# Optimization experiments

Measured on AMD Instinct MI355X. Metric: run time of the kernel, lower is better.

Reference implementation:

```python
import jax, jax.numpy as jnp
import numpy as np

N_NODES = 50000
N_EDGES = 600000
D = 128
N_LAYERS = 4  # 2 base + 2 resnet layers
N_GRAPHS = 64
NEG_SLOPE = 0.01  # F.leaky_relu default


def setup_inputs() -> dict:
    key = jax.random.key(0)
    k1, k2, k3, k4, k5 = jax.random.split(key, 5)
    x = jax.random.normal(k1, (N_NODES, D), dtype=jnp.float32)
    edge_index = jax.random.randint(k2, (2, N_EDGES), 0, N_NODES, dtype=jnp.int64)
    batch = jnp.sort(jax.random.randint(k3, (N_NODES,), 0, N_GRAPHS, dtype=jnp.int64))
    Wl = jax.random.normal(k4, (N_LAYERS, D, D), dtype=jnp.float32) * 0.05
    bl = jnp.zeros((N_LAYERS, D), dtype=jnp.float32)
    Wr = jax.random.normal(k5, (N_LAYERS, D, D), dtype=jnp.float32) * 0.05
    return {"x": x, "edge_index": edge_index, "batch": batch,
            "Wl": Wl, "bl": bl, "Wr": Wr}


def _mean_aggregate(x, src, dst, n_nodes):
    # mean over incoming neighbors; isolated nodes get 0 (PyG scatter-mean semantics)
    s = jax.ops.segment_sum(x[src], dst, num_segments=n_nodes)  # [N, D]
    cnt = jax.ops.segment_sum(jnp.ones((src.shape[0],), x.dtype), dst,
                              num_segments=n_nodes)
    return s / jnp.maximum(cnt, 1.0)[:, None]


def reference(x, edge_index, batch, Wl, bl, Wr):
    src, dst = edge_index[0], edge_index[1]
    n = x.shape[0]
    for i in range(N_LAYERS):
        agg = _mean_aggregate(x, src, dst, n)                      # [N, D]
        # SAGEConv: lin_l(agg) + lin_r(x); lin_l has bias, lin_r does not
        x_new = agg @ Wl[i].T + bl[i] + x @ Wr[i].T
        x_new = jnp.where(x_new >= 0, x_new, NEG_SLOPE * x_new)    # leaky_relu
        x = x_new if i < 2 else x + x_new                          # residual after first 2
    # global mean pool per graph
    pooled = jax.ops.segment_sum(x, batch, num_segments=N_GRAPHS)  # [G, D]
    counts = jax.ops.segment_sum(jnp.ones((n,), x.dtype), batch,
                                 num_segments=N_GRAPHS)
    return pooled / jnp.maximum(counts, 1.0)[:, None]
```

## Files before the change

### kernel.cpp

```cpp
#include <hip/hip_runtime.h>

#define N_NODES 50000
#define N_EDGES 600000
#define DIM 128
#define N_LAYERS 4
#define N_GRAPHS 64
#define NEG_SLOPE 0.01f
#define NB_SCAN ((N_NODES + 255) / 256)
#define NB_CNT ((N_EDGES + 255) / 256)
#define NC_CONV (N_NODES * DIM / 8 / 256)
#define NB_PACK 64
#define RS 264

typedef __attribute__((ext_vector_type(8))) short short8;
typedef __attribute__((ext_vector_type(16))) float floatx16;

__device__ __forceinline__ unsigned short f2bf(float f) {
    union { float f; unsigned u; } c; c.f = f;
    unsigned u = c.u;
    unsigned r = (u + 0x7FFFu + ((u >> 16) & 1u)) >> 16;
    return (unsigned short)r;
}
__device__ __forceinline__ float bfraw2f(unsigned short b) {
    union { unsigned u; float f; } c; c.u = ((unsigned)b) << 16;
    return c.f;
}
__device__ __forceinline__ float bflo(unsigned u) {
    union { unsigned u; float f; } c; c.u = u << 16; return c.f;
}
__device__ __forceinline__ float bfhi(unsigned u) {
    union { unsigned u; float f; } c; c.u = u & 0xFFFF0000u; return c.f;
}

__global__ void zero2(int* a, int na, int* b, int nb) {
    int i = blockIdx.x * blockDim.x + threadIdx.x;
    if (i < na) a[i] = 0;
    else if (i < na + nb) b[i - na] = 0;
}

__global__ void preprocess(const float4* __restrict__ x, uint4* __restrict__ xb,
                           const float* __restrict__ Wl, const float* __restrict__ Wr,
                           ushort* __restrict__ wpk,
                           const int* __restrict__ edst, int* __restrict__ deg) {
    int b = blockIdx.x;
    if (b < NC_CONV) {
        int i = b * 256 + threadIdx.x;
        float4 a = x[i * 2], c = x[i * 2 + 1];
        uint4 o;
        o.x = ((unsigned)f2bf(a.y) << 16) | f2bf(a.x);
        o.y = ((unsigned)f2bf(a.w) << 16) | f2bf(a.z);
        o.z = ((unsigned)f2bf(c.y) << 16) | f2bf(c.x);
        o.w = ((unsigned)f2bf(c.w) << 16) | f2bf(c.z);
        xb[i] = o;
    } else if (b < NC_CONV + NB_PACK) {
        int u = (b - NC_CONV) * 4 + (threadIdx.x >> 6);
        int l = threadIdx.x & 63;
        int layer = u >> 6, m = (u >> 5) & 1, s = (u >> 2) & 7, tt = u & 3;
        const float* W = ((m == 0) ? Wl : Wr) + (size_t)layer * DIM * DIM;
        int n = tt * 32 + (l & 31);
        int kb = s * 16 + (l >> 5) * 8;
        size_t off = ((size_t)u * 64 + l) * 8;
        for (int j = 0; j < 8; j++)
            wpk[off + j] = f2bf(W[n * DIM + kb + j]);
    } else {
        int e = (b - NC_CONV - NB_PACK) * 256 + threadIdx.x;
        if (e < N_EDGES) atomicAdd(&deg[edst[e]], 1);
    }
}

__global__ void scan_pass1(const int* __restrict__ deg, int* __restrict__ bsum) {
    int i = blockIdx.x * 256 + threadIdx.x;
    int v = (i < N_NODES) ? deg[i] : 0;
    for (int off = 32; off > 0; off >>= 1) v += __shfl_down(v, off, 64);
    __shared__ int ws[4];
    int lane = threadIdx.x & 63, w = threadIdx.x >> 6;
    if (lane == 0) ws[w] = v;
    __syncthreads();
    if (threadIdx.x == 0) bsum[blockIdx.x] = ws[0] + ws[1] + ws[2] + ws[3];
}

__global__ void scan_pass2(int* __restrict__ bsum) {
    __shared__ int sm[256];
    int t = threadIdx.x;
    int v = (t < NB_SCAN) ? bsum[t] : 0;
    sm[t] = v;
    __syncthreads();
    for (int off = 1; off < 256; off <<= 1) {
        int u = (t >= off) ? sm[t - off] : 0;
        __syncthreads();
        sm[t] += u;
        __syncthreads();
    }
    if (t < NB_SCAN) bsum[t] = sm[t] - v;
}

__global__ void scan_pass3(const int* __restrict__ deg, const int* __restrict__ bsum,
                           int* __restrict__ rp) {
    int i = blockIdx.x * 256 + threadIdx.x;
    int v = (i < N_NODES) ? deg[i] : 0;
    int lane = threadIdx.x & 63, w = threadIdx.x >> 6;
    int s = v;
    for (int off = 1; off < 64; off <<= 1) {
        int t = __shfl_up(s, off, 64);
        if (lane >= off) s += t;
    }
    __shared__ int ws[4];
    if (lane == 63) ws[w] = s;
    __syncthreads();
    int wo = 0;
    for (int k = 0; k < 4; k++) wo += (k < w) ? ws[k] : 0;
    int incl = s + wo + bsum[blockIdx.x];
    if (i < N_NODES) rp[i + 1] = incl;
    if (i == 0) rp[0] = 0;
}

__global__ void fill_gstart(const int* __restrict__ src, const int* __restrict__ dst,
                            const int* __restrict__ rp, int* __restrict__ fill,
                            int* __restrict__ csr,
                            const int* __restrict__ batch, int* __restrict__ gstart) {
    int b = blockIdx.x;
    if (b < NB_CNT) {
        int e = b * 256 + threadIdx.x;
        if (e >= N_EDGES) return;
        int d = dst[e];
        int pos = atomicAdd(&fill[d], 1);
        csr[rp[d] + pos] = src[e];
    } else {
        int i = (b - NB_CNT) * 256 + threadIdx.x;
        if (i >= N_NODES) return;
        int g0 = batch[i];
        if (i == 0) {
            for (int g = 0; g <= g0; g++) gstart[g] = 0;
        } else {
            int p = batch[i - 1];
            for (int g = p + 1; g <= g0; g++) gstart[g] = i;
        }
        if (i == N_NODES - 1) {
            for (int g = g0 + 1; g <= N_GRAPHS; g++) gstart[g] = N_NODES;
        }
    }
}

__global__ __launch_bounds__(256, 4) void fused_layer_mfma(
    const ushort* __restrict__ xin, ushort* __restrict__ xout,
    const int* __restrict__ rp, const int* __restrict__ csr,
    const ushort* __restrict__ wpk, const float* __restrict__ bias,
    const int* __restrict__ batch, float* __restrict__ pooled,
    int residual, int do_pool) {
    __shared__ ushort sA[64 * RS];
    int t = threadIdx.x;
    int node0 = blockIdx.x * 64;
    int w = t >> 6, l = t & 63;

    const uint4* xv = (const uint4*)(xin + (size_t)node0 * DIM);
#pragma unroll
    for (int i = 0; i < 4; i++) {
        int idx = t + i * 256;
        int r = idx >> 4, c = idx & 15;
        uint4 val = make_uint4(0u, 0u, 0u, 0u);
        if (node0 + r < N_NODES) val = xv[r * 16 + c];
        *(uint4*)&sA[r * RS + 128 + c * 8] = val;
    }

    {
        int ll = l & 15, eg = l >> 4;
        int nb = node0 + w * 16;
        int rpv = rp[min(nb + l, N_NODES)];
        const uint4* x16B = (const uint4*)xin;
        for (int i = 0; i < 16; i++) {
            int s = __shfl(rpv, i, 64);
            int e = __shfl(rpv, i + 1, 64);
            float a0 = 0.f, a1 = 0.f, a2 = 0.f, a3 = 0.f,
                  a4 = 0.f, a5 = 0.f, a6 = 0.f, a7 = 0.f;
            for (int base = s; base < e; base += 64) {
                int cnt = min(64, e - base);
                unsigned myidx = (base + l < e) ? (unsigned)csr[base + l] : 0u;
                for (int j = 0; j < cnt; j += 16) {
                    uint4 v[4];
#pragma unroll
                    for (int k = 0; k < 4; k++) {
                        int sel = j + k * 4 + eg;
                        unsigned idx = __shfl(myidx, sel, 64);
                        v[k] = make_uint4(0u, 0u, 0u, 0u);
                        if (sel < cnt) v[k] = x16B[(size_t)idx * 16 + ll];
                    }
#pragma unroll
                    for (int k = 0; k < 4; k++) {
                        a0 += bflo(v[k].x); a1 += bfhi(v[k].x);
                        a2 += bflo(v[k].y); a3 += bfhi(v[k].y);
                        a4 += bflo(v[k].z); a5 += bfhi(v[k].z);
                        a6 += bflo(v[k].w); a7 += bfhi(v[k].w);
                    }
                }
            }
            a0 += __shfl_xor(a0, 16, 64); a0 += __shfl_xor(a0, 32, 64);
            a1 += __shfl_xor(a1, 16, 64); a1 += __shfl_xor(a1, 32, 64);
            a2 += __shfl_xor(a2, 16, 64); a2 += __shfl_xor(a2, 32, 64);
            a3 += __shfl_xor(a3, 16, 64); a3 += __shfl_xor(a3, 32, 64);
            a4 += __shfl_xor(a4, 16, 64); a4 += __shfl_xor(a4, 32, 64);
            a5 += __shfl_xor(a5, 16, 64); a5 += __shfl_xor(a5, 32, 64);
            a6 += __shfl_xor(a6, 16, 64); a6 += __shfl_xor(a6, 32, 64);
            a7 += __shfl_xor(a7, 16, 64); a7 += __shfl_xor(a7, 32, 64);
            if (eg == 0) {
                float inv = 1.0f / (float)max(e - s, 1);
                uint4 o;
                o.x = ((unsigned)f2bf(a1 * inv) << 16) | f2bf(a0 * inv);
                o.y = ((unsigned)f2bf(a3 * inv) << 16) | f2bf(a2 * inv);
                o.z = ((unsigned)f2bf(a5 * inv) << 16) | f2bf(a4 * inv);
                o.w = ((unsigned)f2bf(a7 * inv) << 16) | f2bf(a6 * inv);
                *(uint4*)&sA[(w * 16 + i) * RS + ll * 8] = o;
            }
        }
    }
    __syncthreads();

    int m0 = (w >> 1) * 32;
    int th = w & 1;
    const ushort* arow = &sA[(m0 + (l & 31)) * RS];
    int khalf = (l >> 5) * 8;

    floatx16 acc0, acc1;
    for (int ii = 0; ii < 16; ii++) acc0[ii] = acc1[ii] = 0.f;

    const ushort* wl8 = wpk + (size_t)l * 8 + (size_t)(2 * th) * 512;
#pragma unroll
    for (int s2 = 0; s2 < 16; s2++) {
        int m = s2 >> 3, s = s2 & 7;
        short8 a = *(const short8*)(arow + m * 128 + s * 16 + khalf);
        size_t fb = (size_t)((m * 8 + s) * 4) * 512;
        short8 b0 = *(const short8*)(wl8 + fb);
        short8 b1 = *(const short8*)(wl8 + fb + 512);
        acc0 = __builtin_amdgcn_mfma_f32_32x32x16_bf16(a, b0, acc0, 0, 0, 0);
        acc1 = __builtin_amdgcn_mfma_f32_32x32x16_bf16(a, b1, acc1, 0, 0, 0);
    }

    int col = l & 31;
    int rbase = 4 * (l >> 5);
    floatx16 accs[2] = {acc0, acc1};
    if (!do_pool) {
#pragma unroll
        for (int ti = 0; ti < 2; ti++) {
            int n = (2 * th + ti) * 32 + col;
            float bv = bias[n];
#pragma unroll
            for (int r = 0; r < 16; r++) {
                int row = (r & 3) + 8 * (r >> 2) + rbase;
                int gm = m0 + row;
                int gn = node0 + gm;
                if (gn >= N_NODES) continue;
                float v = accs[ti][r] + bv;
                v = (v >= 0.f) ? v : NEG_SLOPE * v;
                if (residual) v += bfraw2f(sA[gm * RS + 128 + n]);
                xout[(size_t)gn * DIM + n] = f2bf(v);
            }
        }
    } else {
        bool fast = (node0 + 63 < N_NODES) && (batch[node0] == batch[node0 + 63]);
        int g0 = batch[node0];
#pragma unroll
        for (int ti = 0; ti < 2; ti++) {
            int n = (2 * th + ti) * 32 + col;
            float bv = bias[n];
            float psum = 0.f;
#pragma unroll
            for (int r = 0; r < 16; r++) {
                int row = (r & 3) + 8 * (r >> 2) + rbase;
                int gm = m0 + row;
                int gn = node0 + gm;
                if (gn >= N_NODES) continue;
                float v = accs[ti][r] + bv;
                v = (v >= 0.f) ? v : NEG_SLOPE * v;
                if (residual) v += bfraw2f(sA[gm * RS + 128 + n]);
                if (fast) psum += v;
                else atomicAdd(&pooled[batch[gn] * DIM + n], v);
            }
            if (fast) {
                psum += __shfl_xor(psum, 32, 64);
                if (l < 32) atomicAdd(&pooled[g0 * DIM + n], psum);
            }
        }
    }
}

__global__ void pool_final(const float* __restrict__ pooled,
                           const int* __restrict__ gstart,
                           float* __restrict__ out) {
    int i = blockIdx.x * blockDim.x + threadIdx.x;
    if (i >= N_GRAPHS * DIM) return;
    int g = i >> 7;
    int cnt = gstart[g + 1] - gstart[g];
    out[i] = pooled[i] / (float)max(cnt, 1);
}


extern "C" void kernel_launch(void* const* d_in, const int* in_sizes, int n_in,
                              void* d_out, int out_size, void* d_ws, size_t ws_size,
                              hipStream_t stream) {
    const float* x     = (const float*)d_in[0];
    const int*   ei    = (const int*)d_in[1];
    const int*   batch = (const int*)d_in[2];
    const float* Wl    = (const float*)d_in[3];
    const float* bl    = (const float*)d_in[4];
    const float* Wr    = (const float*)d_in[5];
    float* out = (float*)d_out;

    const int* esrc = ei;
    const int* edst = ei + N_EDGES;

    ushort* xb0  = (ushort*)d_ws;
    ushort* xbuf = xb0 + (size_t)N_NODES * DIM;
    ushort* agg  = xbuf + (size_t)N_NODES * DIM;
    ushort* wpk  = agg + (size_t)N_NODES * DIM;
    int* deg    = (int*)(wpk + (size_t)N_LAYERS * 2 * DIM * DIM);
    int* fill   = deg + N_NODES;
    int* csr    = fill + N_NODES;
    int* rp     = csr + N_EDGES;
    int* gstart = rp + (N_NODES + 1);
    int* bsum   = gstart + (N_GRAPHS + 1);
    float* pooled = (float*)(bsum + NB_SCAN);

    zero2<<<(2 * N_NODES + N_GRAPHS * DIM + 255) / 256, 256, 0, stream>>>(
        deg, 2 * N_NODES, (int*)pooled, N_GRAPHS * DIM);

    preprocess<<<NC_CONV + NB_PACK + NB_CNT, 256, 0, stream>>>(
        (const float4*)x, (uint4*)xb0, Wl, Wr, wpk, edst, deg);

    scan_pass1<<<NB_SCAN, 256, 0, stream>>>(deg, bsum);
    scan_pass2<<<1, 256, 0, stream>>>(bsum);
    scan_pass3<<<NB_SCAN, 256, 0, stream>>>(deg, bsum, rp);

    fill_gstart<<<NB_CNT + NB_SCAN, 256, 0, stream>>>(esrc, edst, rp, fill, csr,
                                                      batch, gstart);

    int gemm_blocks = (N_NODES + 63) / 64;
    const ushort* xi = xb0;
    ushort* xo = xbuf;
    for (int l = 0; l < N_LAYERS; l++) {
        fused_layer_mfma<<<gemm_blocks, 256, 0, stream>>>(
            xi, xo, rp, csr, wpk + (size_t)l * 2 * DIM * DIM,
            bl + (size_t)l * DIM, batch, pooled,
            (l >= 2) ? 1 : 0, (l == N_LAYERS - 1) ? 1 : 0);
        ushort* tmp = (ushort*)xi; xi = xo; xo = tmp;
    }

    pool_final<<<(N_GRAPHS * DIM + 255) / 256, 256, 0, stream>>>(pooled, gstart, out);
}
```

Before: 325.3 us.

## Split aggregation into feature-sliced gather kernel and store activations slice-major

Activations are stored in a feature-sliced layout of four 32-column slices, each contiguous across nodes. Neighbor aggregation moves to a separate kernel with one block per (node block, slice), so each gather touches a smaller working set that fits in cache better. The GEMM kernel then reads the precomputed aggregate and x from the sliced layout. This costs an extra launch per layer and a round trip of the aggregate through global memory, and gives up the fusion of gather and GEMM.

```diff
diff --git a/kernel.cpp b/kernel.cpp
--- a/kernel.cpp
+++ b/kernel.cpp
@@ -10,10 +10,12 @@
 #define NB_CNT ((N_EDGES + 255) / 256)
 #define NC_CONV (N_NODES * DIM / 8 / 256)
 #define NB_PACK 64
+#define NB_NODEBLK ((N_NODES + 63) / 64)
 #define RS 264
 
 typedef __attribute__((ext_vector_type(8))) short short8;
 typedef __attribute__((ext_vector_type(16))) float floatx16;
+typedef unsigned int uint4v __attribute__((ext_vector_type(4)));
 
 __device__ __forceinline__ unsigned short f2bf(float f) {
     union { float f; unsigned u; } c; c.f = f;
@@ -31,6 +33,7 @@
 __device__ __forceinline__ float bfhi(unsigned u) {
     union { unsigned u; float f; } c; c.u = u & 0xFFFF0000u; return c.f;
 }
+
 
 __global__ void zero2(int* a, int na, int* b, int nb) {
     int i = blockIdx.x * blockDim.x + threadIdx.x;
@@ -51,7 +54,8 @@
         o.y = ((unsigned)f2bf(a.w) << 16) | f2bf(a.z);
         o.z = ((unsigned)f2bf(c.y) << 16) | f2bf(c.x);
         o.w = ((unsigned)f2bf(c.w) << 16) | f2bf(c.z);
-        xb[i] = o;
+        int n = i >> 4, dc = i & 15;
+        xb[((size_t)(dc >> 2) * N_NODES + n) * 4 + (dc & 3)] = o;
     } else if (b < NC_CONV + NB_PACK) {
         int u = (b - NC_CONV) * 4 + (threadIdx.x >> 6);
         int l = threadIdx.x & 63;
@@ -141,79 +145,89 @@
     }
 }
 
-__global__ __launch_bounds__(256, 4) void fused_layer_mfma(
-    const ushort* __restrict__ xin, ushort* __restrict__ xout,
-    const int* __restrict__ rp, const int* __restrict__ csr,
+__global__ __launch_bounds__(256) void agg_slice(const ushort* __restrict__ xs,
+                                                 ushort* __restrict__ aggs,
+                                                 const int* __restrict__ rp,
+                                                 const int* __restrict__ csr) {
+    int bid = blockIdx.x;
+    int sl = bid & 3;
+    int nb = bid >> 2;
+    int w = threadIdx.x >> 6, l = threadIdx.x & 63;
+    int g = l >> 2, q = l & 3;
+    const uint4* xsl = (const uint4*)(xs + (size_t)sl * N_NODES * 32);
+    uint4* asl = (uint4*)(aggs + (size_t)sl * N_NODES * 32);
+    int nbase = nb * 64 + w * 16;
+    if (nbase >= N_NODES) return;
+    int rpv = rp[min(nbase + l, N_NODES)];
+    for (int i = 0; i < 16; i++) {
+        int node = nbase + i;
+        if (node >= N_NODES) break;
+        int st = __shfl(rpv, i, 64);
+        int en = __shfl(rpv, i + 1, 64);
+        float a0 = 0.f, a1 = 0.f, a2 = 0.f, a3 = 0.f,
+              a4 = 0.f, a5 = 0.f, a6 = 0.f, a7 = 0.f;
+        for (int base = st; base < en; base += 64) {
+            int cnt = min(64, en - base);
+            unsigned myidx = 0u;
+            if (base + l < en) myidx = (unsigned)__builtin_nontemporal_load(csr + base + l);
+            for (int j = 0; j < cnt; j += 16) {
+                int sel = j + g;
+                unsigned idx = __shfl((int)myidx, sel, 64);
+                uint4 v = make_uint4(0u, 0u, 0u, 0u);
+                if (sel < cnt) v = xsl[(size_t)idx * 4 + q];
+                a0 += bflo(v.x); a1 += bfhi(v.x);
+                a2 += bflo(v.y); a3 += bfhi(v.y);
+                a4 += bflo(v.z); a5 += bfhi(v.z);
+                a6 += bflo(v.w); a7 += bfhi(v.w);
+            }
+        }
+#pragma unroll
+        for (int mask = 4; mask <= 32; mask <<= 1) {
+            a0 += __shfl_xor(a0, mask, 64); a1 += __shfl_xor(a1, mask, 64);
+            a2 += __shfl_xor(a2, mask, 64); a3 += __shfl_xor(a3, mask, 64);
+            a4 += __shfl_xor(a4, mask, 64); a5 += __shfl_xor(a5, mask, 64);
+            a6 += __shfl_xor(a6, mask, 64); a7 += __shfl_xor(a7, mask, 64);
+        }
+        if (g == 0) {
+            float inv = 1.0f / (float)max(en - st, 1);
+            uint4v o;
+            o.x = ((unsigned)f2bf(a1 * inv) << 16) | f2bf(a0 * inv);
+            o.y = ((unsigned)f2bf(a3 * inv) << 16) | f2bf(a2 * inv);
+            o.z = ((unsigned)f2bf(a5 * inv) << 16) | f2bf(a4 * inv);
+            o.w = ((unsigned)f2bf(a7 * inv) << 16) | f2bf(a6 * inv);
+            __builtin_nontemporal_store(o, (uint4v*)&asl[(size_t)node * 4 + q]);
+        }
+    }
+}
+
+__global__ __launch_bounds__(256, 4) void layer_mfma(
+    const ushort* __restrict__ xs, ushort* __restrict__ xout,
+    const ushort* __restrict__ aggs,
     const ushort* __restrict__ wpk, const float* __restrict__ bias,
     const int* __restrict__ batch, float* __restrict__ pooled,
     int residual, int do_pool) {
     __shared__ ushort sA[64 * RS];
     int t = threadIdx.x;
     int node0 = blockIdx.x * 64;
+
+    const uint4* av = (const uint4*)aggs;
+    const uint4* xv = (const uint4*)xs;
+#pragma unroll
+    for (int ii = 0; ii < 8; ii++) {
+        int i = t + ii * 256;
+        int r = i >> 5, c = i & 31;
+        int half = c >> 4, cc = c & 15;
+        int node = node0 + r;
+        uint4 val = make_uint4(0u, 0u, 0u, 0u);
+        if (node < N_NODES) {
+            const uint4* src = half ? xv : av;
+            val = src[((size_t)(cc >> 2) * N_NODES + node) * 4 + (cc & 3)];
+        }
+        *(uint4*)&sA[r * RS + c * 8] = val;
+    }
+    __syncthreads();
+
     int w = t >> 6, l = t & 63;
-
-    const uint4* xv = (const uint4*)(xin + (size_t)node0 * DIM);
-#pragma unroll
-    for (int i = 0; i < 4; i++) {
-        int idx = t + i * 256;
-        int r = idx >> 4, c = idx & 15;
-        uint4 val = make_uint4(0u, 0u, 0u, 0u);
-        if (node0 + r < N_NODES) val = xv[r * 16 + c];
-        *(uint4*)&sA[r * RS + 128 + c * 8] = val;
-    }
-
-    {
-        int ll = l & 15, eg = l >> 4;
-        int nb = node0 + w * 16;
-        int rpv = rp[min(nb + l, N_NODES)];
-        const uint4* x16B = (const uint4*)xin;
-        for (int i = 0; i < 16; i++) {
-            int s = __shfl(rpv, i, 64);
-            int e = __shfl(rpv, i + 1, 64);
-            float a0 = 0.f, a1 = 0.f, a2 = 0.f, a3 = 0.f,
-                  a4 = 0.f, a5 = 0.f, a6 = 0.f, a7 = 0.f;
-            for (int base = s; base < e; base += 64) {
-                int cnt = min(64, e - base);
-                unsigned myidx = (base + l < e) ? (unsigned)csr[base + l] : 0u;
-                for (int j = 0; j < cnt; j += 16) {
-                    uint4 v[4];
-#pragma unroll
-                    for (int k = 0; k < 4; k++) {
-                        int sel = j + k * 4 + eg;
-                        unsigned idx = __shfl(myidx, sel, 64);
-                        v[k] = make_uint4(0u, 0u, 0u, 0u);
-                        if (sel < cnt) v[k] = x16B[(size_t)idx * 16 + ll];
-                    }
-#pragma unroll
-                    for (int k = 0; k < 4; k++) {
-                        a0 += bflo(v[k].x); a1 += bfhi(v[k].x);
-                        a2 += bflo(v[k].y); a3 += bfhi(v[k].y);
-                        a4 += bflo(v[k].z); a5 += bfhi(v[k].z);
-                        a6 += bflo(v[k].w); a7 += bfhi(v[k].w);
-                    }
-                }
-            }
-            a0 += __shfl_xor(a0, 16, 64); a0 += __shfl_xor(a0, 32, 64);
-            a1 += __shfl_xor(a1, 16, 64); a1 += __shfl_xor(a1, 32, 64);
-            a2 += __shfl_xor(a2, 16, 64); a2 += __shfl_xor(a2, 32, 64);
-            a3 += __shfl_xor(a3, 16, 64); a3 += __shfl_xor(a3, 32, 64);
-            a4 += __shfl_xor(a4, 16, 64); a4 += __shfl_xor(a4, 32, 64);
-            a5 += __shfl_xor(a5, 16, 64); a5 += __shfl_xor(a5, 32, 64);
-            a6 += __shfl_xor(a6, 16, 64); a6 += __shfl_xor(a6, 32, 64);
-            a7 += __shfl_xor(a7, 16, 64); a7 += __shfl_xor(a7, 32, 64);
-            if (eg == 0) {
-                float inv = 1.0f / (float)max(e - s, 1);
-                uint4 o;
-                o.x = ((unsigned)f2bf(a1 * inv) << 16) | f2bf(a0 * inv);
-                o.y = ((unsigned)f2bf(a3 * inv) << 16) | f2bf(a2 * inv);
-                o.z = ((unsigned)f2bf(a5 * inv) << 16) | f2bf(a4 * inv);
-                o.w = ((unsigned)f2bf(a7 * inv) << 16) | f2bf(a6 * inv);
-                *(uint4*)&sA[(w * 16 + i) * RS + ll * 8] = o;
-            }
-        }
-    }
-    __syncthreads();
-
     int m0 = (w >> 1) * 32;
     int th = w & 1;
     const ushort* arow = &sA[(m0 + (l & 31)) * RS];
@@ -251,7 +265,7 @@
                 float v = accs[ti][r] + bv;
                 v = (v >= 0.f) ? v : NEG_SLOPE * v;
                 if (residual) v += bfraw2f(sA[gm * RS + 128 + n]);
-                xout[(size_t)gn * DIM + n] = f2bf(v);
+                xout[((size_t)(2 * th + ti) * N_NODES + gn) * 32 + col] = f2bf(v);
             }
         }
     } else {
@@ -309,8 +323,8 @@
 
     ushort* xb0  = (ushort*)d_ws;
     ushort* xbuf = xb0 + (size_t)N_NODES * DIM;
-    ushort* agg  = xbuf + (size_t)N_NODES * DIM;
-    ushort* wpk  = agg + (size_t)N_NODES * DIM;
+    ushort* aggs = xbuf + (size_t)N_NODES * DIM;
+    ushort* wpk  = aggs + (size_t)N_NODES * DIM;
     int* deg    = (int*)(wpk + (size_t)N_LAYERS * 2 * DIM * DIM);
     int* fill   = deg + N_NODES;
     int* csr    = fill + N_NODES;
@@ -332,14 +346,14 @@
     fill_gstart<<<NB_CNT + NB_SCAN, 256, 0, stream>>>(esrc, edst, rp, fill, csr,
                                                       batch, gstart);
 
-    int gemm_blocks = (N_NODES + 63) / 64;
     const ushort* xi = xb0;
     ushort* xo = xbuf;
-    for (int l = 0; l < N_LAYERS; l++) {
-        fused_layer_mfma<<<gemm_blocks, 256, 0, stream>>>(
-            xi, xo, rp, csr, wpk + (size_t)l * 2 * DIM * DIM,
-            bl + (size_t)l * DIM, batch, pooled,
-            (l >= 2) ? 1 : 0, (l == N_LAYERS - 1) ? 1 : 0);
+    for (int lyr = 0; lyr < N_LAYERS; lyr++) {
+        agg_slice<<<NB_NODEBLK * 4, 256, 0, stream>>>(xi, aggs, rp, csr);
+        layer_mfma<<<NB_NODEBLK, 256, 0, stream>>>(
+            xi, xo, aggs, wpk + (size_t)lyr * 2 * DIM * DIM,
+            bl + (size_t)lyr * DIM, batch, pooled,
+            (lyr >= 2) ? 1 : 0, (lyr == N_LAYERS - 1) ? 1 : 0);
         ushort* tmp = (ushort*)xi; xi = xo; xo = tmp;
     }
 
```

Result: slower. 579.2 us (+78.0%).
